# Kernel tuning notes

Measured on AMD Instinct MI355X. Metric: run time of the kernel, lower is better.

The kernel has to match this reference:

```python
import jax, jax.numpy as jnp
import numpy as np

B, C, N, H, W = 8, 128, 16, 56, 56
HID, OUT = 128, 128


def conv1x1(x, w, b):
    # 1x1x1 Conv3d == channel-mixing GEMM. x: [B,Cin,N,H,W], w: [Cout,Cin], b: [Cout]
    return jnp.einsum('oc,bcnhw->bonhw', w, x) + b[None, :, None, None, None]


def setup_inputs() -> dict:
    key = jax.random.key(0)
    ks = jax.random.split(key, 9)
    s = 0.02
    return {
        'x': jax.random.normal(ks[0], (B, C, N, H, W), dtype=jnp.float32),
        'w_q': jax.random.normal(ks[1], (HID, C), dtype=jnp.float32) * s,
        'b_q': jax.random.normal(ks[2], (HID,), dtype=jnp.float32) * s,
        'w_k': jax.random.normal(ks[3], (HID, C), dtype=jnp.float32) * s,
        'b_k': jax.random.normal(ks[4], (HID,), dtype=jnp.float32) * s,
        'w_v': jax.random.normal(ks[5], (HID, C), dtype=jnp.float32) * s,
        'b_v': jax.random.normal(ks[6], (HID,), dtype=jnp.float32) * s,
        'w_o': jax.random.normal(ks[7], (OUT, HID), dtype=jnp.float32) * s,
        'b_o': jax.random.normal(ks[8], (OUT,), dtype=jnp.float32) * s,
    }


def reference(x, w_q, b_q, w_k, b_k, w_v, b_v, w_o, b_o):
    Bsz, Cc, Nn, Hh, Ww = x.shape
    L = Nn * Hh * Ww
    q = conv1x1(x, w_q, b_q).reshape(Bsz, -1, L)   # [B, hid, L]
    k = conv1x1(x, w_k, b_k).reshape(Bsz, -1, L)   # [B, hid, L]
    v = conv1x1(x, w_v, b_v).reshape(Bsz, -1, L)   # [B, hid, L]
    # NOTE: attention is over CHANNELS (hid x hid), since k was transposed to [B, L, hid]
    attn = jax.nn.softmax(jnp.einsum('bql,bkl->bqk', q, k), axis=-1)  # [B, hid, hid]
    feats = jnp.einsum('bqk,bkl->bql', attn, v).reshape(Bsz, -1, Nn, Hh, Ww)
    out = conv1x1(feats, w_o, b_o) + x             # residual requires out_dim == in_dim
    return jnp.mean(out, axis=2)                   # mean over N (depth) -> [B, out, H, W]
```

## Files before the change

kernel.cpp:

```cpp
#include <hip/hip_runtime.h>
#include <hip/hip_bf16.h>
#include <cstdint>

#define BB   8
#define CCH  128
#define NND  16
#define HWD  3136
#define LLT  50176
#define HWB  32
#define NHB  98
#define K3WB 64
#define K3NB 49

#define OFF_SP  0
#define OFF_RP  12845056
#define OFF_S   12945408
#define OFF_M   13076480
#define OFF_Q   13207552
#define OFF_AV  13338624
#define OFF_CV  13339648

typedef __attribute__((ext_vector_type(8)))  short bf16x8;
typedef __attribute__((ext_vector_type(16))) float f32x16;

__device__ __forceinline__ uint32_t fbits(float f){ union{float f;uint32_t u;}v; v.f=f; return v.u; }
__device__ __forceinline__ float bitsf(uint32_t u){ union{uint32_t u;float f;}v; v.u=u; return v.f; }

#define MFMA32(a,b,c) __builtin_amdgcn_mfma_f32_32x32x16_bf16((a),(b),(c),0,0,0)

#define BARRIER_KEEP_VMEM() do{                                  \
    asm volatile("s_waitcnt lgkmcnt(0)" ::: "memory");           \
    __builtin_amdgcn_s_barrier();                                \
  }while(0)

__global__ __launch_bounds__(256,3) void k1_gram(const float* __restrict__ x,
    float* __restrict__ Sp, float* __restrict__ rp, float* __restrict__ Y)
{
  __shared__ __align__(16) short lds_h[2][4*129*8];
  __shared__ __align__(16) short lds_l[2][4*129*8];
  const int b   = blockIdx.x / NHB;
  const int hb  = blockIdx.x % NHB;
  const int hw0 = hb * HWB;
  const int tid = threadIdx.x;
  const int lane = tid & 63, w = tid >> 6;
  const int wr = w >> 1, wc = w & 1;
  const int cr = tid >> 3;
  const int p  = tid & 7;
  const int kc = p >> 1, hf = p & 1;
  const float* xb = x + (size_t)b*CCH*LLT + (size_t)cr*LLT + hw0 + 4*p;

  f32x16 acc[2][2];
  #pragma unroll
  for(int ai=0;ai<2;ai++)
    #pragma unroll
    for(int bi=0;bi<2;bi++)
      #pragma unroll
      for(int e=0;e<16;e++) acc[ai][bi][e] = 0.f;
  float yac[16];
  #pragma unroll
  for(int i=0;i<16;i++) yac[i]=0.f;

  float4 vA[4], vB[4];

#define LOADP(VV, nn)                                                       \
  { _Pragma("unroll")                                                       \
    for(int j=0;j<4;j++)                                                    \
      VV[j] = *(const float4*)(xb + (size_t)(32*j)*LLT + (size_t)(nn)*HWD); }

#define SPLIT(bufi, VV)                                                     \
  {                                                                         \
    _Pragma("unroll")                                                       \
    for(int j=0;j<4;j++){                                                   \
      const int c = 32*j + cr;                                              \
      const float x0=VV[j].x, x1=VV[j].y, x2=VV[j].z, x3=VV[j].w;           \
      const uint32_t a0=fbits(x0),a1=fbits(x1),a2=fbits(x2),a3=fbits(x3);   \
      const int h0 = __builtin_amdgcn_perm(a1, a0, 0x07060302u);            \
      const int h1 = __builtin_amdgcn_perm(a3, a2, 0x07060302u);            \
      const float l0 = x0 - bitsf(a0&0xFFFF0000u);                          \
      const float l1 = x1 - bitsf(a1&0xFFFF0000u);                          \
      const float l2 = x2 - bitsf(a2&0xFFFF0000u);                          \
      const float l3 = x3 - bitsf(a3&0xFFFF0000u);                          \
      const int g0 = __builtin_amdgcn_perm(fbits(l1), fbits(l0), 0x07060302u); \
      const int g1 = __builtin_amdgcn_perm(fbits(l3), fbits(l2), 0x07060302u); \
      const int sa = (kc*129 + c)*8 + 4*hf;                                 \
      *(int2*)&lds_h[bufi][sa] = make_int2(h0,h1);                          \
      *(int2*)&lds_l[bufi][sa] = make_int2(g0,g1);                          \
      yac[4*j+0]+=x0; yac[4*j+1]+=x1; yac[4*j+2]+=x2; yac[4*j+3]+=x3;       \
    }                                                                       \
  }

#define COMPUTE(bufi)                                                       \
  { _Pragma("unroll")                                                       \
    for(int ks=0;ks<2;ks++){                                                \
      const int kk = 2*ks + (lane>>5);                                      \
      const int rbase = (kk*129 + (lane&31))*8;                             \
      const bf16x8 a0h = *(const bf16x8*)&lds_h[bufi][rbase + (64*wr    )*8]; \
      const bf16x8 a0l = *(const bf16x8*)&lds_l[bufi][rbase + (64*wr    )*8]; \
      const bf16x8 a1h = *(const bf16x8*)&lds_h[bufi][rbase + (64*wr+32)*8]; \
      const bf16x8 a1l = *(const bf16x8*)&lds_l[bufi][rbase + (64*wr+32)*8]; \
      const bf16x8 b0h = *(const bf16x8*)&lds_h[bufi][rbase + (64*wc    )*8]; \
      const bf16x8 b0l = *(const bf16x8*)&lds_l[bufi][rbase + (64*wc    )*8]; \
      const bf16x8 b1h = *(const bf16x8*)&lds_h[bufi][rbase + (64*wc+32)*8]; \
      const bf16x8 b1l = *(const bf16x8*)&lds_l[bufi][rbase + (64*wc+32)*8]; \
      acc[0][0] = MFMA32(a0h, b0h, acc[0][0]);                              \
      acc[0][0] = MFMA32(a0h, b0l, acc[0][0]);                              \
      acc[0][0] = MFMA32(a0l, b0h, acc[0][0]);                              \
      acc[0][1] = MFMA32(a0h, b1h, acc[0][1]);                              \
      acc[0][1] = MFMA32(a0h, b1l, acc[0][1]);                              \
      acc[0][1] = MFMA32(a0l, b1h, acc[0][1]);                              \
      acc[1][0] = MFMA32(a1h, b0h, acc[1][0]);                              \
      acc[1][0] = MFMA32(a1h, b0l, acc[1][0]);                              \
      acc[1][0] = MFMA32(a1l, b0h, acc[1][0]);                              \
      acc[1][1] = MFMA32(a1h, b1h, acc[1][1]);                              \
      acc[1][1] = MFMA32(a1h, b1l, acc[1][1]);                              \
      acc[1][1] = MFMA32(a1l, b1h, acc[1][1]);                              \
    } }

  LOADP(vA, 0);
  LOADP(vB, 1);
  SPLIT(0, vA);
  LOADP(vA, 2);
  BARRIER_KEEP_VMEM();

  for(int n2=0;n2<NND/2;n2++){
    const int n = 2*n2;
    COMPUTE(0);
    SPLIT(1, vB);
    if(n+3<NND) LOADP(vB, n+3);
    BARRIER_KEEP_VMEM();
    COMPUTE(1);
    if(n+2<NND){
      SPLIT(0, vA);
      if(n+4<NND) LOADP(vA, n+4);
    }
    BARRIER_KEEP_VMEM();
  }
#undef COMPUTE
#undef SPLIT
#undef LOADP

  #pragma unroll
  for(int j=0;j<4;j++){
    float4 o4 = make_float4(yac[4*j]*0.0625f, yac[4*j+1]*0.0625f,
                            yac[4*j+2]*0.0625f, yac[4*j+3]*0.0625f);
    *(float4*)(Y + ((size_t)b*CCH + 32*j + cr)*HWD + hw0 + 4*p) = o4;
  }
  #pragma unroll
  for(int j=0;j<4;j++){
    float s = yac[4*j]+yac[4*j+1]+yac[4*j+2]+yac[4*j+3];
    #pragma unroll
    for(int st=1;st<8;st<<=1) s += __shfl_xor(s, st, 8);
    if(p==0) rp[(size_t)(b*NHB+hb)*CCH + 32*j + cr] = s;
  }

  float* Sb = Sp + (size_t)(b*NHB+hb)*CCH*CCH;
  const int col = lane & 31, roff = 4*(lane>>5);
  #pragma unroll
  for(int ai=0;ai<2;ai++)
    #pragma unroll
    for(int bi=0;bi<2;bi++)
      #pragma unroll
      for(int reg=0;reg<16;reg++){
        const int row = 64*wr + 32*ai + roff + (reg&3) + 8*(reg>>2);
        Sb[(size_t)row*CCH + 64*wc + 32*bi + col] = acc[ai][bi][reg];
      }
}

__global__ __launch_bounds__(256) void k1r(const float* __restrict__ Sp,
                                           float* __restrict__ S)
{
  const int b  = blockIdx.x >> 4;
  const int ch = blockIdx.x & 15;
  const int i  = ch*1024 + threadIdx.x*4;
  const float* p = Sp + (size_t)b*NHB*CCH*CCH + i;
  float4 s = make_float4(0.f,0.f,0.f,0.f);
  for(int hb=0;hb<NHB;hb++){
    float4 v = *(const float4*)(p + (size_t)hb*CCH*CCH);
    s.x+=v.x; s.y+=v.y; s.z+=v.z; s.w+=v.w;
  }
  *(float4*)(S + (size_t)b*CCH*CCH + i) = s;
}

__global__ __launch_bounds__(256) void k2ab(const float* __restrict__ S, const float* __restrict__ rp,
    const float* __restrict__ wq, const float* __restrict__ bq,
    const float* __restrict__ wk, const float* __restrict__ bk,
    const float* __restrict__ wv, const float* __restrict__ bv,
    float* __restrict__ M, float* __restrict__ av)
{
  __shared__ __align__(16) float t1[16][132];
  __shared__ float rb_s[CCH];
  __shared__ float wrk_s[CCH];
  __shared__ float wrq_s[16];
  const int b   = blockIdx.x >> 3;
  const int r0  = (blockIdx.x & 7) * 16;
  const int tid = threadIdx.x;
  const float* Sb = S + (size_t)b*CCH*CCH;

  if(tid < CCH){
    float s = 0.f;
    const float* rpb = rp + (size_t)b*NHB*CCH + tid;
    for(int hb=0;hb<NHB;hb++) s += rpb[hb*CCH];
    rb_s[tid] = s;
  }
  __syncthreads();

  if(tid < CCH){
    float s = 0.f;
    for(int m=0;m<CCH;m++) s += wk[(size_t)tid*CCH+m]*rb_s[m];
    wrk_s[tid] = s;
  } else if(tid < CCH+16){
    const int rr2 = tid - CCH;
    float s = 0.f;
    for(int m=0;m<CCH;m++) s += wq[(size_t)(r0+rr2)*CCH+m]*rb_s[m];
    wrq_s[rr2] = s;
  }

  const int rr = tid >> 4;
  const int c0 = (tid & 15) * 8;
  {
    float a8[8] = {0,0,0,0,0,0,0,0};
    const float* wqr = wq + (size_t)(r0+rr)*CCH;
    for(int m4=0;m4<32;m4++){
      float4 w4 = *(const float4*)(wqr + 4*m4);
      const float wl[4] = {w4.x,w4.y,w4.z,w4.w};
      #pragma unroll
      for(int mm=0;mm<4;mm++){
        const int m = 4*m4+mm;
        const float w = wl[mm];
        float4 s0 = *(const float4*)(Sb + (size_t)m*CCH + c0);
        float4 s1 = *(const float4*)(Sb + (size_t)m*CCH + c0 + 4);
        a8[0]=fmaf(w,s0.x,a8[0]); a8[1]=fmaf(w,s0.y,a8[1]);
        a8[2]=fmaf(w,s0.z,a8[2]); a8[3]=fmaf(w,s0.w,a8[3]);
        a8[4]=fmaf(w,s1.x,a8[4]); a8[5]=fmaf(w,s1.y,a8[5]);
        a8[6]=fmaf(w,s1.z,a8[6]); a8[7]=fmaf(w,s1.w,a8[7]);
      }
    }
    #pragma unroll
    for(int j=0;j<8;j++) t1[rr][c0+j] = a8[j];
  }
  __syncthreads();

  const int j0 = c0;
  float g[8] = {0,0,0,0,0,0,0,0};
  for(int c4=0;c4<32;c4++){
    float4 tv = *(const float4*)(&t1[rr][4*c4]);
    #pragma unroll
    for(int jj=0;jj<8;jj++){
      float4 w4 = *(const float4*)(wk + (size_t)(j0+jj)*CCH + 4*c4);
      g[jj]=fmaf(tv.x,w4.x,g[jj]); g[jj]=fmaf(tv.y,w4.y,g[jj]);
      g[jj]=fmaf(tv.z,w4.z,g[jj]); g[jj]=fmaf(tv.w,w4.w,g[jj]);
    }
  }
  const float bqr  = bq[r0+rr];
  const float wrqr = wrq_s[rr];
  #pragma unroll
  for(int jj=0;jj<8;jj++)
    g[jj] += wrqr*bk[j0+jj] + bqr*wrk_s[j0+jj] + (float)LLT*bqr*bk[j0+jj];

  float mx = g[0];
  #pragma unroll
  for(int jj=1;jj<8;jj++) mx = fmaxf(mx, g[jj]);
  #pragma unroll
  for(int s=1;s<16;s<<=1) mx = fmaxf(mx, __shfl_xor(mx, s, 16));
  float ex[8], sum=0.f;
  #pragma unroll
  for(int jj=0;jj<8;jj++){ ex[jj] = expf(g[jj]-mx); sum += ex[jj]; }
  #pragma unroll
  for(int s=1;s<16;s<<=1) sum += __shfl_xor(sum, s, 16);
  const float inv = 1.0f/sum;

  float pa = 0.f;
  #pragma unroll
  for(int jj=0;jj<8;jj++) pa += ex[jj]*inv*bv[j0+jj];
  #pragma unroll
  for(int s=1;s<16;s<<=1) pa += __shfl_xor(pa, s, 16);
  if((tid&15)==0) av[b*CCH + r0+rr] = pa;

  __syncthreads();
  #pragma unroll
  for(int jj=0;jj<8;jj++) t1[rr][j0+jj] = ex[jj]*inv;
  __syncthreads();

  {
    float a8[8] = {0,0,0,0,0,0,0,0};
    for(int k4=0;k4<32;k4++){
      float4 a4 = *(const float4*)(&t1[rr][4*k4]);
      const float al[4] = {a4.x,a4.y,a4.z,a4.w};
      #pragma unroll
      for(int kk=0;kk<4;kk++){
        const int k = 4*k4+kk;
        const float wgt = al[kk];
        float4 v0 = *(const float4*)(wv + (size_t)k*CCH + c0);
        float4 v1 = *(const float4*)(wv + (size_t)k*CCH + c0 + 4);
        a8[0]=fmaf(wgt,v0.x,a8[0]); a8[1]=fmaf(wgt,v0.y,a8[1]);
        a8[2]=fmaf(wgt,v0.z,a8[2]); a8[3]=fmaf(wgt,v0.w,a8[3]);
        a8[4]=fmaf(wgt,v1.x,a8[4]); a8[5]=fmaf(wgt,v1.y,a8[5]);
        a8[6]=fmaf(wgt,v1.z,a8[6]); a8[7]=fmaf(wgt,v1.w,a8[7]);
      }
    }
    float* Mr = M + ((size_t)b*CCH + r0+rr)*CCH + c0;
    *(float4*)(Mr  ) = make_float4(a8[0],a8[1],a8[2],a8[3]);
    *(float4*)(Mr+4) = make_float4(a8[4],a8[5],a8[6],a8[7]);
  }
}

__global__ __launch_bounds__(256) void k2c(const float* __restrict__ M,
    const float* __restrict__ wo, const float* __restrict__ bo,
    const float* __restrict__ av, float* __restrict__ Q, float* __restrict__ cv)
{
  const int b  = blockIdx.x >> 3;
  const int o0 = (blockIdx.x & 7)*16;
  const int tid = threadIdx.x;
  const int rr = tid>>4, c0 = (tid&15)*8;
  const int o  = o0 + rr;
  const float* wor = wo + (size_t)o*CCH;
  const float* Mb  = M + (size_t)b*CCH*CCH;
  float a8[8] = {0,0,0,0,0,0,0,0};
  for(int m4=0;m4<32;m4++){
    float4 w4 = *(const float4*)(wor + 4*m4);
    const float wl[4] = {w4.x,w4.y,w4.z,w4.w};
    #pragma unroll
    for(int mm=0;mm<4;mm++){
      const int m = 4*m4+mm;
      const float w = wl[mm];
      float4 v0 = *(const float4*)(Mb + (size_t)m*CCH + c0);
      float4 v1 = *(const float4*)(Mb + (size_t)m*CCH + c0 + 4);
      a8[0]=fmaf(w,v0.x,a8[0]); a8[1]=fmaf(w,v0.y,a8[1]);
      a8[2]=fmaf(w,v0.z,a8[2]); a8[3]=fmaf(w,v0.w,a8[3]);
      a8[4]=fmaf(w,v1.x,a8[4]); a8[5]=fmaf(w,v1.y,a8[5]);
      a8[6]=fmaf(w,v1.z,a8[6]); a8[7]=fmaf(w,v1.w,a8[7]);
    }
  }
  #pragma unroll
  for(int j=0;j<8;j++) if(o == c0+j) a8[j] += 1.0f;
  float* Qr = Q + ((size_t)b*CCH + o)*CCH + c0;
  *(float4*)(Qr  ) = make_float4(a8[0],a8[1],a8[2],a8[3]);
  *(float4*)(Qr+4) = make_float4(a8[4],a8[5],a8[6],a8[7]);

  if(tid < 16){
    const int oo = o0 + tid;
    float s = 0.f;
    for(int m=0;m<CCH;m++) s += wo[(size_t)oo*CCH+m]*av[b*CCH+m];
    cv[b*CCH + oo] = s + bo[oo];
  }
}

__global__ __launch_bounds__(256,2) void k3(const float* __restrict__ Q,
    const float* __restrict__ cv, float* __restrict__ out)
{
  __shared__ __align__(16) float4 qs[4096];
  const int b   = blockIdx.x / K3NB;
  const int hb  = blockIdx.x % K3NB;
  const int hw0 = hb * K3WB;
  const int tid = threadIdx.x;

  const float4* Qg = (const float4*)(Q + (size_t)b*CCH*CCH);
  #pragma unroll
  for(int it=0; it<16; it++){
    const int idx = it*256 + tid;
    const int row = idx >> 5, ch = idx & 31;
    qs[(row<<5) | (ch ^ (row>>3))] = Qg[idx];
  }
  __syncthreads();

  const int tx = tid & 15, ty = tid >> 4;
  const int o0 = tx*8;
  const int hg = ty*4;
  float acc[8][4];
  #pragma unroll
  for(int i=0;i<8;i++){ acc[i][0]=0.f; acc[i][1]=0.f; acc[i][2]=0.f; acc[i][3]=0.f; }

  const float* Yb = out + (size_t)b*CCH*HWD + hw0 + hg;
  for(int c4=0;c4<32;c4++){
    float4 yv[4];
    #pragma unroll
    for(int mm=0;mm<4;mm++) yv[mm] = *(const float4*)(Yb + (size_t)(4*c4+mm)*HWD);
    #pragma unroll
    for(int i=0;i<8;i++){
      const int row = o0 + i;
      const float4 q4 = qs[(row<<5) | (c4 ^ tx)];
      const float ql[4] = {q4.x,q4.y,q4.z,q4.w};
      #pragma unroll
      for(int mm=0;mm<4;mm++){
        acc[i][0]=fmaf(ql[mm],yv[mm].x,acc[i][0]);
        acc[i][1]=fmaf(ql[mm],yv[mm].y,acc[i][1]);
        acc[i][2]=fmaf(ql[mm],yv[mm].z,acc[i][2]);
        acc[i][3]=fmaf(ql[mm],yv[mm].w,acc[i][3]);
      }
    }
  }
  __syncthreads();
  #pragma unroll
  for(int i=0;i<8;i++){
    const float c = cv[b*CCH + o0+i];
    float4 o4 = make_float4(acc[i][0]+c, acc[i][1]+c, acc[i][2]+c, acc[i][3]+c);
    *(float4*)(out + ((size_t)b*CCH + o0+i)*HWD + hw0 + hg) = o4;
  }
}

extern "C" void kernel_launch(void* const* d_in, const int* in_sizes, int n_in,
                              void* d_out, int out_size, void* d_ws, size_t ws_size,
                              hipStream_t stream) {
  const float* x  = (const float*)d_in[0];
  const float* wq = (const float*)d_in[1];
  const float* bq = (const float*)d_in[2];
  const float* wk = (const float*)d_in[3];
  const float* bk = (const float*)d_in[4];
  const float* wv = (const float*)d_in[5];
  const float* bv = (const float*)d_in[6];
  const float* wo = (const float*)d_in[7];
  const float* bo = (const float*)d_in[8];
  float* out = (float*)d_out;
  float* ws  = (float*)d_ws;

  k1_gram<<<BB*NHB, 256, 0, stream>>>(x, ws+OFF_SP, ws+OFF_RP, out);
  k1r<<<128, 256, 0, stream>>>(ws+OFF_SP, ws+OFF_S);
  k2ab<<<64, 256, 0, stream>>>(ws+OFF_S, ws+OFF_RP, wq, bq, wk, bk, wv, bv,
                               ws+OFF_M, ws+OFF_AV);
  k2c<<<64, 256, 0, stream>>>(ws+OFF_M, wo, bo, ws+OFF_AV, ws+OFF_Q, ws+OFF_CV);
  k3<<<BB*K3NB, 256, 0, stream>>>(ws+OFF_Q, ws+OFF_CV, out);
}
```

Baseline: 171.2 us.

## Prepack x into split-bf16 MFMA layout and accumulate Gram via atomics

Adds a pack kernel that converts x once into hi/lo bf16 planes in an MFMA-friendly transposed layout, and a streaming Gram kernel that reads the packed data and accumulates S and row sums with atomicAdd. This replaces the per-block partial Gram buffers and the separate k1r reduction pass. The packed copy costs an extra full write and read of x-sized data, and the atomics make the summation order nondeterministic. The new path runs only when the workspace is large enough, otherwise the old path is kept.

```diff
diff --git a/kernel.cpp b/kernel.cpp
--- a/kernel.cpp
+++ b/kernel.cpp
@@ -20,11 +20,22 @@
 #define OFF_AV  13338624
 #define OFF_CV  13339648
 
+#define OFF2_XPH 0
+#define OFF2_XPL 25690112
+#define OFF2_S   51380224
+#define OFF2_R   51511296
+#define OFF2_M   51512320
+#define OFF2_Q   51643392
+#define OFF2_AV  51774464
+#define OFF2_CV  51775488
+#define NEED2_BYTES ((size_t)51776512*4)
+
 typedef __attribute__((ext_vector_type(8)))  short bf16x8;
 typedef __attribute__((ext_vector_type(16))) float f32x16;
 
 __device__ __forceinline__ uint32_t fbits(float f){ union{float f;uint32_t u;}v; v.f=f; return v.u; }
 __device__ __forceinline__ float bitsf(uint32_t u){ union{uint32_t u;float f;}v; v.u=u; return v.f; }
+__device__ __forceinline__ float bf2f(unsigned short u){ return bitsf(((uint32_t)u)<<16); }
 
 #define MFMA32(a,b,c) __builtin_amdgcn_mfma_f32_32x32x16_bf16((a),(b),(c),0,0,0)
 
@@ -32,6 +43,158 @@
     asm volatile("s_waitcnt lgkmcnt(0)" ::: "memory");           \
     __builtin_amdgcn_s_barrier();                                \
   }while(0)
+
+
+__global__ __launch_bounds__(256,2) void kT_pack(const float* __restrict__ x,
+    unsigned short* __restrict__ xPh, unsigned short* __restrict__ xPl,
+    float* __restrict__ S, float* __restrict__ r)
+{
+  __shared__ __align__(16) unsigned short sh[28*33*8];
+  __shared__ __align__(16) unsigned short sl[28*33*8];
+  const int blk = blockIdx.x;
+  const int n  = blk & 15;
+  const int cg = (blk >> 4) & 3;
+  const int b  = blk >> 6;
+  const int tid = threadIdx.x;
+  const int cl = tid >> 3;
+  const int p  = tid & 7;
+
+  S[blk*256 + tid] = 0.f;
+  if(blk < 4) r[blk*256 + tid] = 0.f;
+
+  const float* xr = x + (size_t)(b*CCH + cg*32 + cl)*LLT + n*HWD;
+
+  float4 v[7];
+  #pragma unroll
+  for(int s=0;s<7;s++) v[s] = *(const float4*)(xr + 4*p + 32*s);
+
+  for(int t=0; t<14; t++){
+    #pragma unroll
+    for(int s=0;s<7;s++){
+      const float x0=v[s].x, x1=v[s].y, x2=v[s].z, x3=v[s].w;
+      const uint32_t a0=fbits(x0),a1=fbits(x1),a2=fbits(x2),a3=fbits(x3);
+      const int h0 = __builtin_amdgcn_perm(a1, a0, 0x07060302u);
+      const int h1 = __builtin_amdgcn_perm(a3, a2, 0x07060302u);
+      const float l0 = x0 - bitsf(a0&0xFFFF0000u);
+      const float l1 = x1 - bitsf(a1&0xFFFF0000u);
+      const float l2 = x2 - bitsf(a2&0xFFFF0000u);
+      const float l3 = x3 - bitsf(a3&0xFFFF0000u);
+      const int g0 = __builtin_amdgcn_perm(fbits(l1), fbits(l0), 0x07060302u);
+      const int g1 = __builtin_amdgcn_perm(fbits(l3), fbits(l2), 0x07060302u);
+      const int lcl = (p>>1) + 4*s;
+      const int sa = (lcl*33 + cl)*8 + 4*(p&1);
+      *(int2*)&sh[sa] = make_int2(h0,h1);
+      *(int2*)&sl[sa] = make_int2(g0,g1);
+    }
+    BARRIER_KEEP_VMEM();
+    if(t+1 < 14){
+      #pragma unroll
+      for(int s=0;s<7;s++) v[s] = *(const float4*)(xr + 224*(t+1) + 4*p + 32*s);
+    }
+    #pragma unroll
+    for(int i=0;i<7;i++){
+      const int pc = i*256 + tid;
+      const int c  = pc & 31;
+      const int rr = pc >> 5;
+      const int lcl = (rr<28) ? rr : rr-28;
+      const size_t go = ((size_t)(b*6272 + n*392 + 28*t + lcl)*128 + cg*32 + c)*8;
+      const int4 val = *(const int4*)&((rr<28)? sh : sl)[(lcl*33 + c)*8];
+      if(rr<28) *(int4*)&xPh[go] = val;
+      else      *(int4*)&xPl[go] = val;
+    }
+    BARRIER_KEEP_VMEM();
+  }
+}
+
+__global__ __launch_bounds__(256,3) void kG_stream(
+    const unsigned short* __restrict__ xPh, const unsigned short* __restrict__ xPl,
+    float* __restrict__ S, float* __restrict__ r, float* __restrict__ Y)
+{
+  const int jp = blockIdx.x % 98;
+  const int b  = blockIdx.x / 98;
+  const int tid = threadIdx.x, lane = tid & 63, w = tid >> 6;
+  const int wr = w >> 1, wc = w & 1;
+  const int hh = lane >> 5, cli = lane & 31;
+
+  f32x16 acc[2][2];
+  #pragma unroll
+  for(int ai=0;ai<2;ai++)
+    #pragma unroll
+    for(int bi=0;bi<2;bi++)
+      #pragma unroll
+      for(int e=0;e<16;e++) acc[ai][bi][e] = 0.f;
+  float yac[2][8];
+  #pragma unroll
+  for(int q=0;q<2;q++)
+    #pragma unroll
+    for(int e=0;e<8;e++) yac[q][e] = 0.f;
+
+  const size_t base = (size_t)b*6272*1024;
+  for(int n=0;n<NND;n++){
+    const size_t rb = base + (size_t)(n*392 + 4*jp)*1024;
+    #pragma unroll
+    for(int qp=0;qp<2;qp++){
+      const size_t r0 = rb + (size_t)(2*qp + hh)*1024;
+      const bf16x8 a0h = *(const bf16x8*)&xPh[r0 + (64*wr      + cli)*8];
+      const bf16x8 a0l = *(const bf16x8*)&xPl[r0 + (64*wr      + cli)*8];
+      const bf16x8 a1h = *(const bf16x8*)&xPh[r0 + (64*wr + 32 + cli)*8];
+      const bf16x8 a1l = *(const bf16x8*)&xPl[r0 + (64*wr + 32 + cli)*8];
+      const bf16x8 b0h = *(const bf16x8*)&xPh[r0 + (64*wc      + cli)*8];
+      const bf16x8 b0l = *(const bf16x8*)&xPl[r0 + (64*wc      + cli)*8];
+      const bf16x8 b1h = *(const bf16x8*)&xPh[r0 + (64*wc + 32 + cli)*8];
+      const bf16x8 b1l = *(const bf16x8*)&xPl[r0 + (64*wc + 32 + cli)*8];
+      acc[0][0] = MFMA32(a0h, b0h, acc[0][0]);
+      acc[0][0] = MFMA32(a0h, b0l, acc[0][0]);
+      acc[0][0] = MFMA32(a0l, b0h, acc[0][0]);
+      acc[0][1] = MFMA32(a0h, b1h, acc[0][1]);
+      acc[0][1] = MFMA32(a0h, b1l, acc[0][1]);
+      acc[0][1] = MFMA32(a0l, b1h, acc[0][1]);
+      acc[1][0] = MFMA32(a1h, b0h, acc[1][0]);
+      acc[1][0] = MFMA32(a1h, b0l, acc[1][0]);
+      acc[1][0] = MFMA32(a1l, b0h, acc[1][0]);
+      acc[1][1] = MFMA32(a1h, b1h, acc[1][1]);
+      acc[1][1] = MFMA32(a1h, b1l, acc[1][1]);
+      acc[1][1] = MFMA32(a1l, b1h, acc[1][1]);
+      const bf16x8 ych = wc ? a1h : a0h;
+      const bf16x8 ycl = wc ? a1l : a0l;
+      #pragma unroll
+      for(int e=0;e<8;e++)
+        yac[qp][e] += bf2f((unsigned short)ych[e]) + bf2f((unsigned short)ycl[e]);
+    }
+  }
+
+  const int c = 64*wr + 32*wc + cli;
+  #pragma unroll
+  for(int qp=0;qp<2;qp++){
+    const int hw = (4*jp + 2*qp + hh)*8;
+    float4 o0 = make_float4(yac[qp][0]*0.0625f, yac[qp][1]*0.0625f,
+                            yac[qp][2]*0.0625f, yac[qp][3]*0.0625f);
+    float4 o1 = make_float4(yac[qp][4]*0.0625f, yac[qp][5]*0.0625f,
+                            yac[qp][6]*0.0625f, yac[qp][7]*0.0625f);
+    *(float4*)(Y + ((size_t)b*CCH + c)*HWD + hw    ) = o0;
+    *(float4*)(Y + ((size_t)b*CCH + c)*HWD + hw + 4) = o1;
+  }
+  float rs = 0.f;
+  #pragma unroll
+  for(int qp=0;qp<2;qp++)
+    #pragma unroll
+    for(int e=0;e<8;e++) rs += yac[qp][e];
+  rs += __shfl_xor(rs, 32);
+  if(hh==0) atomicAdd(&r[b*CCH + c], rs);
+
+  float* Sb = S + (size_t)b*CCH*CCH;
+  const int roff = 4*hh;
+  #pragma unroll
+  for(int ai=0;ai<2;ai++)
+    #pragma unroll
+    for(int bi=0;bi<2;bi++)
+      #pragma unroll
+      for(int reg=0;reg<16;reg++){
+        const int row = 64*wr + 32*ai + roff + (reg&3) + 8*(reg>>2);
+        atomicAdd(&Sb[(size_t)row*CCH + 64*wc + 32*bi + cli], acc[ai][bi][reg]);
+      }
+}
+
 
 __global__ __launch_bounds__(256,3) void k1_gram(const float* __restrict__ x,
     float* __restrict__ Sp, float* __restrict__ rp, float* __restrict__ Y)
@@ -167,25 +330,26 @@
 }
 
 __global__ __launch_bounds__(256) void k1r(const float* __restrict__ Sp,
-                                           float* __restrict__ S)
+                                           float* __restrict__ S, int nparts)
 {
   const int b  = blockIdx.x >> 4;
   const int ch = blockIdx.x & 15;
   const int i  = ch*1024 + threadIdx.x*4;
-  const float* p = Sp + (size_t)b*NHB*CCH*CCH + i;
+  const float* p = Sp + (size_t)b*nparts*CCH*CCH + i;
   float4 s = make_float4(0.f,0.f,0.f,0.f);
-  for(int hb=0;hb<NHB;hb++){
+  for(int hb=0;hb<nparts;hb++){
     float4 v = *(const float4*)(p + (size_t)hb*CCH*CCH);
     s.x+=v.x; s.y+=v.y; s.z+=v.z; s.w+=v.w;
   }
   *(float4*)(S + (size_t)b*CCH*CCH + i) = s;
 }
+
 
 __global__ __launch_bounds__(256) void k2ab(const float* __restrict__ S, const float* __restrict__ rp,
     const float* __restrict__ wq, const float* __restrict__ bq,
     const float* __restrict__ wk, const float* __restrict__ bk,
     const float* __restrict__ wv, const float* __restrict__ bv,
-    float* __restrict__ M, float* __restrict__ av)
+    float* __restrict__ M, float* __restrict__ av, int nparts)
 {
   __shared__ __align__(16) float t1[16][132];
   __shared__ float rb_s[CCH];
@@ -198,8 +362,8 @@
 
   if(tid < CCH){
     float s = 0.f;
-    const float* rpb = rp + (size_t)b*NHB*CCH + tid;
-    for(int hb=0;hb<NHB;hb++) s += rpb[hb*CCH];
+    const float* rpb = rp + (size_t)b*nparts*CCH + tid;
+    for(int hb=0;hb<nparts;hb++) s += rpb[hb*CCH];
     rb_s[tid] = s;
   }
   __syncthreads();
@@ -413,10 +577,21 @@
   float* out = (float*)d_out;
   float* ws  = (float*)d_ws;
 
-  k1_gram<<<BB*NHB, 256, 0, stream>>>(x, ws+OFF_SP, ws+OFF_RP, out);
-  k1r<<<128, 256, 0, stream>>>(ws+OFF_SP, ws+OFF_S);
-  k2ab<<<64, 256, 0, stream>>>(ws+OFF_S, ws+OFF_RP, wq, bq, wk, bk, wv, bv,
-                               ws+OFF_M, ws+OFF_AV);
-  k2c<<<64, 256, 0, stream>>>(ws+OFF_M, wo, bo, ws+OFF_AV, ws+OFF_Q, ws+OFF_CV);
-  k3<<<BB*K3NB, 256, 0, stream>>>(ws+OFF_Q, ws+OFF_CV, out);
-}
+  if(ws_size >= NEED2_BYTES){
+    unsigned short* xph = (unsigned short*)(ws + OFF2_XPH);
+    unsigned short* xpl = (unsigned short*)(ws + OFF2_XPL);
+    kT_pack  <<<512, 256, 0, stream>>>(x, xph, xpl, ws+OFF2_S, ws+OFF2_R);
+    kG_stream<<<8*98, 256, 0, stream>>>(xph, xpl, ws+OFF2_S, ws+OFF2_R, out);
+    k2ab<<<64, 256, 0, stream>>>(ws+OFF2_S, ws+OFF2_R, wq, bq, wk, bk, wv, bv,
+                                 ws+OFF2_M, ws+OFF2_AV, 1);
+    k2c <<<64, 256, 0, stream>>>(ws+OFF2_M, wo, bo, ws+OFF2_AV, ws+OFF2_Q, ws+OFF2_CV);
+    k3  <<<BB*K3NB, 256, 0, stream>>>(ws+OFF2_Q, ws+OFF2_CV, out);
+  } else {
+    k1_gram<<<BB*NHB, 256, 0, stream>>>(x, ws+OFF_SP, ws+OFF_RP, out);
+    k1r<<<128, 256, 0, stream>>>(ws+OFF_SP, ws+OFF_S, NHB);
+    k2ab<<<64, 256, 0, stream>>>(ws+OFF_S, ws+OFF_RP, wq, bq, wk, bk, wv, bv,
+                                 ws+OFF_M, ws+OFF_AV, NHB);
+    k2c<<<64, 256, 0, stream>>>(ws+OFF_M, wo, bo, ws+OFF_AV, ws+OFF_Q, ws+OFF_CV);
+    k3<<<BB*K3NB, 256, 0, stream>>>(ws+OFF_Q, ws+OFF_CV, out);
+  }
+}
```

New measurement: 261.1 us. +52.5%, slower.
